# Kernel tuning notes

Hardware: AMD Instinct MI355X
Metric: run time of the kernel (lower is better)

The kernel has to match this reference:

```python
import jax, jax.numpy as jnp
import numpy as np
from jax import lax

K = 7            # cfg.network.PSROI_BINS == pool_size
FEAT_STRIDE = 16
LAMDA = 0.1
D_PER_BIN = 8    # feature channels per position-sensitive bin -> C = K*K*8 = 392


def _bilinear(feat, y, x, extra_idx):
    """Bilinearly sample feat[H,W,...] at float coords (y,x); extra_idx are
    integer index arrays (broadcast to y.shape) selecting trailing feat axes."""
    H, W = feat.shape[0], feat.shape[1]
    y0f = jnp.floor(y); x0f = jnp.floor(x)
    wy = (y - y0f)[..., None]
    wx = (x - x0f)[..., None]
    y0 = jnp.clip(y0f.astype(jnp.int32), 0, H - 1)
    y1 = jnp.clip(y0f.astype(jnp.int32) + 1, 0, H - 1)
    x0 = jnp.clip(x0f.astype(jnp.int32), 0, W - 1)
    x1 = jnp.clip(x0f.astype(jnp.int32) + 1, 0, W - 1)
    def g(yi, xi):
        return feat[(yi, xi) + extra_idx]
    return ((1 - wy) * (1 - wx) * g(y0, x0) + (1 - wy) * wx * g(y0, x1)
            + wy * (1 - wx) * g(y1, x0) + wy * wx * g(y1, x1))


def ps_roi(f, rois, k, feat_stride, offsets=None):
    """Position-sensitive RoI pooling. f: [H,W,C] with C = k*k*D (bin-major
    channel layout). rois: [N,5] (batch, x1, y1, x2, y2) in image coords.
    offsets (optional): [N, k*k, G, 2] per-bin, per-channel-group (x,y) shifts
    in image coords. Returns [N, D, k, k]."""
    H, W, C = f.shape
    N = rois.shape[0]
    kk = k * k
    D = C // kk
    x1 = rois[:, 1] / feat_stride
    y1 = rois[:, 2] / feat_stride
    x2 = (rois[:, 3] + 1.0) / feat_stride
    y2 = (rois[:, 4] + 1.0) / feat_stride
    bw = (x2 - x1) / k  # [N]
    bh = (y2 - y1) / k
    jj = jnp.tile(jnp.arange(k, dtype=f.dtype), k)     # bin = i*k + j
    ii = jnp.repeat(jnp.arange(k, dtype=f.dtype), k)
    cx = x1[:, None] + (jj + 0.5) * bw[:, None]        # [N, kk] bin centers
    cy = y1[:, None] + (ii + 0.5) * bh[:, None]
    bins = jnp.arange(kk, dtype=jnp.int32)
    if offsets is None:
        feat = f.reshape(H, W, kk, D)
        b = jnp.broadcast_to(bins, (N, kk))
        vals = _bilinear(feat, cy, cx, (b,))           # [N, kk, D]
    else:
        G = offsets.shape[2]
        cxg = cx[:, :, None] + offsets[..., 0] / feat_stride  # [N, kk, G]
        cyg = cy[:, :, None] + offsets[..., 1] / feat_stride
        feat = f.reshape(H, W, kk, G, D // G)
        b = jnp.broadcast_to(bins[None, :, None], (N, kk, G))
        g = jnp.broadcast_to(jnp.arange(G, dtype=jnp.int32)[None, None, :], (N, kk, G))
        vals = _bilinear(feat, cyg, cxg, (b, g))       # [N, kk, G, D//G]
        vals = vals.reshape(N, kk, D)
    return jnp.transpose(vals.reshape(N, k, k, D), (0, 3, 1, 2))  # [N, D, k, k]


def setup_inputs():
    key = jax.random.key(0)
    kf, kw, k1, k2 = jax.random.split(key, 4)
    H = W = 128
    C = K * K * D_PER_BIN
    N = 2048
    features = jax.random.normal(kf, (1, H, W, C), jnp.float32)
    conv_w = jax.random.normal(kw, (3, 3, C, 2 * 4 * K * K), jnp.float32) * 0.01
    img = float(H * FEAT_STRIDE)
    xy1 = jax.random.uniform(k1, (N, 2), minval=0.0, maxval=img * 0.6)
    wh = jax.random.uniform(k2, (N, 2), minval=32.0, maxval=img * 0.4)
    xy2 = jnp.minimum(xy1 + wh, img - 1.0)
    rois = jnp.concatenate([jnp.zeros((N, 1)), xy1[:, :1], xy1[:, 1:], xy2[:, :1], xy2[:, 1:]], axis=1).astype(jnp.float32)
    return {"features": features, "rois": rois, "conv_w": conv_w}


def reference(features, rois, conv_w):
    # offset branch: 3x3 conv (no bias) -> PS-RoI pool -> scale by lamda*roi size
    offset_map = lax.conv_general_dilated(features, conv_w, (1, 1), 'SAME',
                                          dimension_numbers=('NHWC', 'HWIO', 'NHWC'))
    off = ps_roi(offset_map[0], rois, K, FEAT_STRIDE)          # [N, 8, K, K]
    N = off.shape[0]
    off = off.reshape(N, -1, 2, K, K)                          # [N, 4, 2, K, K]
    off = jnp.transpose(off, (2, 3, 4, 1, 0))                  # [2, K, K, 4, N]
    roi_w = rois[:, 3] - rois[:, 1] + 1.0
    roi_h = rois[:, 4] - rois[:, 2] + 1.0
    off = jnp.stack((off[0] * roi_w * LAMDA, off[1] * roi_h * LAMDA), axis=0)
    off = jnp.transpose(off, (4, 1, 2, 3, 0))                  # [N, K, K, 4, 2]
    off = off.reshape(N, K * K, -1, 2)                         # [N, kk, 4, 2]
    # deformable PS-RoI pooling of the features with predicted offsets
    return ps_roi(features[0], rois, K, FEAT_STRIDE, offsets=off)  # [N, 8, K, K]
```

## Files before the change

### kernel.cpp

```cpp
#include <hip/hip_runtime.h>
#include <cstddef>
#include <cstdint>

#define HH    128
#define WW    128
#define CC    392
#define NPIX  (HH*WW)
#define NROI  2048
#define PSK   7
#define NBIN  49
#define LAMDA 0.1f

#define CPAD      448
#define HPAD      130
#define NPADCO    512
#define SEGSTRIDE (9*CPAD)
#define BKK       64

#define FBM 64
#define FBN 64
#define FBK 32

typedef _Float16 half8   __attribute__((ext_vector_type(8)));
typedef float    floatx4 __attribute__((ext_vector_type(4)));

__device__ __forceinline__ void async_ld16(const _Float16* g, _Float16* l) {
  __builtin_amdgcn_global_load_lds((const __attribute__((address_space(1))) void*)g,
                                   (__attribute__((address_space(3))) void*)l,
                                   16, 0, 0);
}

__global__ __launch_bounds__(256)
void conv_f_kernel(const float* __restrict__ F, _Float16* __restrict__ Fh) {
  const int idx = blockIdx.x * 256 + threadIdx.x;
  const int total = HPAD * HPAD * (CPAD / 8);
  if (idx >= total) return;
  const int p  = idx / (CPAD / 8);
  const int cg = idx - p * (CPAD / 8);
  const int c  = cg * 8;
  const int py = p / HPAD;
  const int px = p - py * HPAD;
  half8 h;
#pragma unroll
  for (int i = 0; i < 8; ++i) h[i] = (_Float16)0.f;
  if (py >= 1 && py <= HH && px >= 1 && px <= WW && c < CC) {
    const float* src = F + ((size_t)(py - 1) * WW + (px - 1)) * CC + c;
    const float4 v0 = *(const float4*)src;
    const float4 v1 = *(const float4*)(src + 4);
    h[0] = (_Float16)v0.x; h[1] = (_Float16)v0.y;
    h[2] = (_Float16)v0.z; h[3] = (_Float16)v0.w;
    h[4] = (_Float16)v1.x; h[5] = (_Float16)v1.y;
    h[6] = (_Float16)v1.z; h[7] = (_Float16)v1.w;
  }
  *(half8*)(Fh + (size_t)p * CPAD + c) = h;
}

__global__ __launch_bounds__(256)
void conv_w_kernel(const float* __restrict__ Wt, _Float16* __restrict__ Bth) {
  __shared__ float tile[32][33];
  const int bid = blockIdx.x;
  const int seg = bid / (14 * 16);
  const int rem = bid - seg * (14 * 16);
  const int cit = rem / 16;
  const int cot = rem - cit * 16;
  const int ci0 = cit * 32, co0 = cot * 32;
  const int t = threadIdx.x;
#pragma unroll
  for (int i = 0; i < 4; ++i) {
    const int idx = t + i * 256;
    const int lr = idx >> 5;
    const int lc = idx & 31;
    const int ci = ci0 + lr, co = co0 + lc;
    float v = 0.f;
    if (ci < CC && co < CC) v = Wt[((size_t)seg * CC + ci) * CC + co];
    tile[lr][lc] = v;
  }
  __syncthreads();
#pragma unroll
  for (int i = 0; i < 4; ++i) {
    const int idx = t + i * 256;
    const int lr = idx >> 5;
    const int lc = idx & 31;
    Bth[(size_t)(co0 + lr) * SEGSTRIDE + seg * CPAD + ci0 + lc] = (_Float16)tile[lc][lr];
  }
}

__global__ __launch_bounds__(256, 2)
void conv_mfma_kernel(const _Float16* __restrict__ Fh, const _Float16* __restrict__ Bth,
                      _Float16* __restrict__ OM) {
  __shared__ __align__(16) _Float16 As[128 * BKK];
  __shared__ __align__(16) _Float16 Bs[128 * BKK];

  const int t = threadIdx.x;
  const int L = t & 63;
  const int w = t >> 6;
  const int row0 = blockIdx.x * 128;
  const int col0 = blockIdx.y * 128;

  const int srow = L >> 3;
  const int kofs = ((L & 7) ^ srow) * 8;

  const int ya = row0 >> 7;
  const int nbase = col0 + w * 32 + srow;

  const int wm = (w >> 1) * 64;
  const int wn = (w & 1) * 64;
  const int fr = L & 15;
  const int quad = L >> 4;
  const int pg0 = (quad ^ (fr & 7)) * 8;
  const int pg1 = ((4 + quad) ^ (fr & 7)) * 8;

  floatx4 acc[4][4];
#pragma unroll
  for (int i = 0; i < 4; ++i)
#pragma unroll
    for (int j = 0; j < 4; ++j) {
      floatx4 z = {0.f, 0.f, 0.f, 0.f};
      acc[i][j] = z;
    }

  for (int seg = 0; seg < 9; ++seg) {
    const int dy = seg / 3 - 1;
    const int dx = seg - (seg / 3) * 3 - 1;
    const int fy = ya + 1 + dy;
    const _Float16* gArow = Fh + ((size_t)fy * HPAD + (1 + dx)) * CPAD + kofs;
    const _Float16* gB = Bth + (size_t)nbase * SEGSTRIDE + seg * CPAD + kofs;

    for (int it = 0; it < 7; ++it) {
      const int cb = it * BKK;
#pragma unroll
      for (int j = 0; j < 4; ++j) {
        const int xr = w * 32 + j * 8 + srow;
        async_ld16(gArow + (size_t)xr * CPAD + cb, &As[(w * 32 + j * 8) * BKK]);
      }
#pragma unroll
      for (int j = 0; j < 4; ++j) {
        async_ld16(gB + (size_t)(j * 8) * SEGSTRIDE + cb, &Bs[(w * 32 + j * 8) * BKK]);
      }
      __syncthreads();

      half8 a0[4], a1[4], b0[4], b1[4];
#pragma unroll
      for (int mt = 0; mt < 4; ++mt) {
        const int rb = (wm + mt * 16 + fr) * BKK;
        a0[mt] = *(const half8*)(&As[rb + pg0]);
        a1[mt] = *(const half8*)(&As[rb + pg1]);
      }
#pragma unroll
      for (int nt = 0; nt < 4; ++nt) {
        const int rb = (wn + nt * 16 + fr) * BKK;
        b0[nt] = *(const half8*)(&Bs[rb + pg0]);
        b1[nt] = *(const half8*)(&Bs[rb + pg1]);
      }
#pragma unroll
      for (int mt = 0; mt < 4; ++mt)
#pragma unroll
        for (int nt = 0; nt < 4; ++nt)
          acc[mt][nt] = __builtin_amdgcn_mfma_f32_16x16x32_f16(a0[mt], b0[nt], acc[mt][nt], 0, 0, 0);
#pragma unroll
      for (int mt = 0; mt < 4; ++mt)
#pragma unroll
        for (int nt = 0; nt < 4; ++nt)
          acc[mt][nt] = __builtin_amdgcn_mfma_f32_16x16x32_f16(a1[mt], b1[nt], acc[mt][nt], 0, 0, 0);
      __syncthreads();
    }
  }

#pragma unroll
  for (int mt = 0; mt < 4; ++mt) {
    const int rbase = row0 + wm + mt * 16 + quad * 4;
#pragma unroll
    for (int nt = 0; nt < 4; ++nt) {
      const int col = col0 + wn + nt * 16 + fr;
      if (col < CC) {
#pragma unroll
        for (int r = 0; r < 4; ++r)
          OM[(size_t)(rbase + r) * CC + col] = (_Float16)acc[mt][nt][r];
      }
    }
  }
}

__global__ __launch_bounds__(256)
void conv3x3_kernel(const float* __restrict__ F, const float* __restrict__ Wt,
                    float* __restrict__ OM) {
  __shared__ float Asf[FBK][FBM + 4];
  __shared__ float Bsf[FBK][FBN + 4];

  const int t = threadIdx.x;
  const int ty = t >> 4;
  const int tx = t & 15;
  const int row0 = blockIdx.x * FBM;
  const int col0 = blockIdx.y * FBN;

  float acc[4][4];
#pragma unroll
  for (int i = 0; i < 4; ++i)
#pragma unroll
    for (int j = 0; j < 4; ++j) acc[i][j] = 0.f;

  for (int kc = 0; kc < 117; ++kc) {
    const int seg   = kc / 13;
    const int cbase = (kc - seg * 13) * FBK;
    const int dy    = seg / 3 - 1;
    const int dx    = seg - (seg / 3) * 3 - 1;

#pragma unroll
    for (int rep = 0; rep < (FBM * FBK) / 256; ++rep) {
      const int idx = t + rep * 256;
      const int r  = idx >> 5;
      const int lk = idx & 31;
      const int m  = row0 + r;
      const int y  = m >> 7, x = m & 127;
      const int yy = y + dy, xx = x + dx;
      const int ci = cbase + lk;
      float v = 0.f;
      if ((unsigned)yy < HH && (unsigned)xx < WW && ci < CC)
        v = F[((size_t)(yy * WW + xx)) * CC + ci];
      Asf[lk][r] = v;
    }
#pragma unroll
    for (int rep = 0; rep < (FBK * FBN) / 256; ++rep) {
      const int idx = t + rep * 256;
      const int lk  = idx >> 6;
      const int nn  = idx & 63;
      const int ci  = cbase + lk;
      const int col = col0 + nn;
      float v = 0.f;
      if (ci < CC && col < CC)
        v = Wt[((size_t)(seg * CC + ci)) * CC + col];
      Bsf[lk][nn] = v;
    }
    __syncthreads();

#pragma unroll
    for (int lk = 0; lk < FBK; ++lk) {
      const float4 a4 = *(const float4*)(&Asf[lk][ty * 4]);
      const float4 b4 = *(const float4*)(&Bsf[lk][tx * 4]);
      const float av[4] = {a4.x, a4.y, a4.z, a4.w};
      const float bv[4] = {b4.x, b4.y, b4.z, b4.w};
#pragma unroll
      for (int i = 0; i < 4; ++i)
#pragma unroll
        for (int j = 0; j < 4; ++j)
          acc[i][j] = fmaf(av[i], bv[j], acc[i][j]);
    }
    __syncthreads();
  }

  const int col = col0 + tx * 4;
  if (col < CC) {
#pragma unroll
    for (int i = 0; i < 4; ++i) {
      float4 v = make_float4(acc[i][0], acc[i][1], acc[i][2], acc[i][3]);
      *(float4*)(&OM[((size_t)(row0 + ty * 4 + i)) * CC + col]) = v;
    }
  }
}

__device__ __forceinline__ void bilin_setup(float y, float x,
                                            int& iy0, int& iy1, int& ix0, int& ix1,
                                            float& w00, float& w01, float& w10, float& w11) {
  const float y0f = floorf(y), x0f = floorf(x);
  const float wy = y - y0f, wx = x - x0f;
  const int a = (int)y0f, b = (int)x0f;
  iy0 = min(max(a, 0), HH - 1);
  iy1 = min(max(a + 1, 0), HH - 1);
  ix0 = min(max(b, 0), WW - 1);
  ix1 = min(max(b + 1, 0), WW - 1);
  w00 = (1.f - wy) * (1.f - wx);
  w01 = (1.f - wy) * wx;
  w10 = wy * (1.f - wx);
  w11 = wy * wx;
}

template <typename TOM>
__global__ __launch_bounds__(256)
void psroi_pool_kernel(const float* __restrict__ F, const float* __restrict__ R,
                       const TOM* __restrict__ OM, float* __restrict__ out) {
  const int tid = blockIdx.x * 256 + threadIdx.x;
  if (tid >= NROI * NBIN * 4) return;
  const int g  = tid & 3;
  const int nb = tid >> 2;
  const int n  = nb / NBIN;
  const int b  = nb - n * NBIN;
  const int bi = b / PSK;
  const int bj = b - bi * PSK;

  const float rx1 = R[n * 5 + 1], ry1 = R[n * 5 + 2];
  const float rx2 = R[n * 5 + 3], ry2 = R[n * 5 + 4];

  const float x1 = rx1 * (1.f / 16.f);
  const float y1 = ry1 * (1.f / 16.f);
  const float x2 = (rx2 + 1.f) * (1.f / 16.f);
  const float y2 = (ry2 + 1.f) * (1.f / 16.f);
  const float bw = (x2 - x1) * (1.f / 7.f);
  const float bh = (y2 - y1) * (1.f / 7.f);
  const float cx = x1 + ((float)bj + 0.5f) * bw;
  const float cy = y1 + ((float)bi + 0.5f) * bh;

  int iy0, iy1, ix0, ix1;
  float w00, w01, w10, w11;
  bilin_setup(cy, cx, iy0, iy1, ix0, ix1, w00, w01, w10, w11);

  const size_t c0 = (size_t)b * 8 + 2 * g;
  const size_t s00 = (size_t)(iy0 * WW + ix0) * CC + c0;
  const size_t s01 = (size_t)(iy0 * WW + ix1) * CC + c0;
  const size_t s10 = (size_t)(iy1 * WW + ix0) * CC + c0;
  const size_t s11 = (size_t)(iy1 * WW + ix1) * CC + c0;

  const float ox = w00 * (float)OM[s00]     + w01 * (float)OM[s01]
                 + w10 * (float)OM[s10]     + w11 * (float)OM[s11];
  const float oy = w00 * (float)OM[s00 + 1] + w01 * (float)OM[s01 + 1]
                 + w10 * (float)OM[s10 + 1] + w11 * (float)OM[s11 + 1];

  const float roiw = rx2 - rx1 + 1.f;
  const float roih = ry2 - ry1 + 1.f;
  const float sx = cx + ox * roiw * (LAMDA / 16.f);
  const float sy = cy + oy * roih * (LAMDA / 16.f);

  int jy0, jy1, jx0, jx1;
  float u00, u01, u10, u11;
  bilin_setup(sy, sx, jy0, jy1, jx0, jx1, u00, u01, u10, u11);

  const float2 q00 = *(const float2*)(F + (size_t)(jy0 * WW + jx0) * CC + c0);
  const float2 q01 = *(const float2*)(F + (size_t)(jy0 * WW + jx1) * CC + c0);
  const float2 q10 = *(const float2*)(F + (size_t)(jy1 * WW + jx0) * CC + c0);
  const float2 q11 = *(const float2*)(F + (size_t)(jy1 * WW + jx1) * CC + c0);

  const float v0 = u00 * q00.x + u01 * q01.x + u10 * q10.x + u11 * q11.x;
  const float v1 = u00 * q00.y + u01 * q01.y + u10 * q10.y + u11 * q11.y;

  out[((size_t)n * 8 + 2 * g + 0) * NBIN + b] = v0;
  out[((size_t)n * 8 + 2 * g + 1) * NBIN + b] = v1;
}

extern "C" void kernel_launch(void* const* d_in, const int* in_sizes, int n_in,
                              void* d_out, int out_size, void* d_ws, size_t ws_size,
                              hipStream_t stream) {
  const float* F  = (const float*)d_in[0];
  const float* R  = (const float*)d_in[1];
  const float* Wt = (const float*)d_in[2];
  float* out = (float*)d_out;

  const size_t omBytes  = (size_t)NPIX * CC * sizeof(_Float16);
  const size_t fhBytes  = (size_t)HPAD * HPAD * CPAD * sizeof(_Float16);
  const size_t bthBytes = (size_t)NPADCO * SEGSTRIDE * sizeof(_Float16);
  const size_t need = omBytes + fhBytes + bthBytes;

  const int totalPool = NROI * NBIN * 4;

  if (ws_size >= need) {
    _Float16* OM  = (_Float16*)d_ws;
    _Float16* Fh  = (_Float16*)((char*)d_ws + omBytes);
    _Float16* Bth = (_Float16*)((char*)d_ws + omBytes + fhBytes);

    const int fTotal = HPAD * HPAD * (CPAD / 8);
    conv_f_kernel<<<(fTotal + 255) / 256, 256, 0, stream>>>(F, Fh);
    conv_w_kernel<<<9 * 14 * 16, 256, 0, stream>>>(Wt, Bth);

    dim3 g(NPIX / 128, NPADCO / 128);
    conv_mfma_kernel<<<g, 256, 0, stream>>>(Fh, Bth, OM);

    psroi_pool_kernel<_Float16><<<(totalPool + 255) / 256, 256, 0, stream>>>(F, R, OM, out);
  } else {
    float* OM = (float*)d_ws;
    dim3 cgrid(NPIX / FBM, (CC + FBN - 1) / FBN);
    conv3x3_kernel<<<cgrid, 256, 0, stream>>>(F, Wt, OM);
    psroi_pool_kernel<float><<<(totalPool + 255) / 256, 256, 0, stream>>>(F, R, OM, out);
  }
}
```

Before: 166.4 us.

## Shrink conv N-tile padding, merge prep kernels, pool from fp16 features

Reduces output-channel padding from 512 to 448 and halves the MFMA tile width to 64 columns, which cuts wasted MMA work and doubles the grid while raising the occupancy hint. It also merges the feature and weight conversion kernels into one launch, flattens the seg/k loops, and makes the pooling kernel read half2 offset values and the fp16 padded feature copy instead of fp32 features. Narrower tiles reduce A-tile reuse per block, and sampling from fp16 features adds rounding error in the final output.

```diff
diff --git a/kernel.cpp b/kernel.cpp
--- a/kernel.cpp
+++ b/kernel.cpp
@@ -13,7 +13,7 @@
 
 #define CPAD      448
 #define HPAD      130
-#define NPADCO    512
+#define NPADCO    448
 #define SEGSTRIDE (9*CPAD)
 #define BKK       64
 
@@ -22,6 +22,7 @@
 #define FBK 32
 
 typedef _Float16 half8   __attribute__((ext_vector_type(8)));
+typedef _Float16 half2v  __attribute__((ext_vector_type(2)));
 typedef float    floatx4 __attribute__((ext_vector_type(4)));
 
 __device__ __forceinline__ void async_ld16(const _Float16* g, _Float16* l) {
@@ -30,147 +31,150 @@
                                    16, 0, 0);
 }
 
+#define FPREP ((HPAD * HPAD * (CPAD / 8) + 255) / 256)
+#define WPREP (9 * 14 * 14)
+
 __global__ __launch_bounds__(256)
-void conv_f_kernel(const float* __restrict__ F, _Float16* __restrict__ Fh) {
-  const int idx = blockIdx.x * 256 + threadIdx.x;
-  const int total = HPAD * HPAD * (CPAD / 8);
-  if (idx >= total) return;
-  const int p  = idx / (CPAD / 8);
-  const int cg = idx - p * (CPAD / 8);
-  const int c  = cg * 8;
-  const int py = p / HPAD;
-  const int px = p - py * HPAD;
-  half8 h;
-#pragma unroll
-  for (int i = 0; i < 8; ++i) h[i] = (_Float16)0.f;
-  if (py >= 1 && py <= HH && px >= 1 && px <= WW && c < CC) {
-    const float* src = F + ((size_t)(py - 1) * WW + (px - 1)) * CC + c;
-    const float4 v0 = *(const float4*)src;
-    const float4 v1 = *(const float4*)(src + 4);
-    h[0] = (_Float16)v0.x; h[1] = (_Float16)v0.y;
-    h[2] = (_Float16)v0.z; h[3] = (_Float16)v0.w;
-    h[4] = (_Float16)v1.x; h[5] = (_Float16)v1.y;
-    h[6] = (_Float16)v1.z; h[7] = (_Float16)v1.w;
-  }
-  *(half8*)(Fh + (size_t)p * CPAD + c) = h;
-}
-
-__global__ __launch_bounds__(256)
-void conv_w_kernel(const float* __restrict__ Wt, _Float16* __restrict__ Bth) {
+void prep_kernel(const float* __restrict__ F, const float* __restrict__ Wt,
+                 _Float16* __restrict__ Fh, _Float16* __restrict__ Bth) {
   __shared__ float tile[32][33];
-  const int bid = blockIdx.x;
-  const int seg = bid / (14 * 16);
-  const int rem = bid - seg * (14 * 16);
-  const int cit = rem / 16;
-  const int cot = rem - cit * 16;
-  const int ci0 = cit * 32, co0 = cot * 32;
   const int t = threadIdx.x;
-#pragma unroll
-  for (int i = 0; i < 4; ++i) {
-    const int idx = t + i * 256;
-    const int lr = idx >> 5;
-    const int lc = idx & 31;
-    const int ci = ci0 + lr, co = co0 + lc;
-    float v = 0.f;
-    if (ci < CC && co < CC) v = Wt[((size_t)seg * CC + ci) * CC + co];
-    tile[lr][lc] = v;
-  }
-  __syncthreads();
-#pragma unroll
-  for (int i = 0; i < 4; ++i) {
-    const int idx = t + i * 256;
-    const int lr = idx >> 5;
-    const int lc = idx & 31;
-    Bth[(size_t)(co0 + lr) * SEGSTRIDE + seg * CPAD + ci0 + lc] = (_Float16)tile[lc][lr];
-  }
-}
-
-__global__ __launch_bounds__(256, 2)
+  if (blockIdx.x < FPREP) {
+    const int idx = blockIdx.x * 256 + t;
+    const int total = HPAD * HPAD * (CPAD / 8);
+    if (idx >= total) return;
+    const int p  = idx / (CPAD / 8);
+    const int cg = idx - p * (CPAD / 8);
+    const int c  = cg * 8;
+    const int py = p / HPAD;
+    const int px = p - py * HPAD;
+    half8 h;
+#pragma unroll
+    for (int i = 0; i < 8; ++i) h[i] = (_Float16)0.f;
+    if (py >= 1 && py <= HH && px >= 1 && px <= WW && c < CC) {
+      const float* src = F + ((size_t)(py - 1) * WW + (px - 1)) * CC + c;
+      const float4 v0 = *(const float4*)src;
+      const float4 v1 = *(const float4*)(src + 4);
+      h[0] = (_Float16)v0.x; h[1] = (_Float16)v0.y;
+      h[2] = (_Float16)v0.z; h[3] = (_Float16)v0.w;
+      h[4] = (_Float16)v1.x; h[5] = (_Float16)v1.y;
+      h[6] = (_Float16)v1.z; h[7] = (_Float16)v1.w;
+    }
+    *(half8*)(Fh + (size_t)p * CPAD + c) = h;
+  } else {
+    const int bid = blockIdx.x - FPREP;
+    const int seg = bid / (14 * 14);
+    const int rem = bid - seg * (14 * 14);
+    const int cit = rem / 14;
+    const int cot = rem - cit * 14;
+    const int ci0 = cit * 32, co0 = cot * 32;
+#pragma unroll
+    for (int i = 0; i < 4; ++i) {
+      const int idx = t + i * 256;
+      const int lr = idx >> 5;
+      const int lc = idx & 31;
+      const int ci = ci0 + lr, co = co0 + lc;
+      float v = 0.f;
+      if (ci < CC && co < CC) v = Wt[((size_t)seg * CC + ci) * CC + co];
+      tile[lr][lc] = v;
+    }
+    __syncthreads();
+#pragma unroll
+    for (int i = 0; i < 4; ++i) {
+      const int idx = t + i * 256;
+      const int lr = idx >> 5;
+      const int lc = idx & 31;
+      Bth[(size_t)(co0 + lr) * SEGSTRIDE + seg * CPAD + ci0 + lc] = (_Float16)tile[lc][lr];
+    }
+  }
+}
+
+__global__ __launch_bounds__(256, 4)
 void conv_mfma_kernel(const _Float16* __restrict__ Fh, const _Float16* __restrict__ Bth,
                       _Float16* __restrict__ OM) {
   __shared__ __align__(16) _Float16 As[128 * BKK];
-  __shared__ __align__(16) _Float16 Bs[128 * BKK];
+  __shared__ __align__(16) _Float16 Bs[64 * BKK];
 
   const int t = threadIdx.x;
   const int L = t & 63;
   const int w = t >> 6;
   const int row0 = blockIdx.x * 128;
-  const int col0 = blockIdx.y * 128;
+  const int col0 = blockIdx.y * 64;
 
   const int srow = L >> 3;
   const int kofs = ((L & 7) ^ srow) * 8;
 
   const int ya = row0 >> 7;
-  const int nbase = col0 + w * 32 + srow;
+  const int nbase = col0 + w * 16 + srow;
 
   const int wm = (w >> 1) * 64;
-  const int wn = (w & 1) * 64;
+  const int wn = (w & 1) * 32;
   const int fr = L & 15;
   const int quad = L >> 4;
   const int pg0 = (quad ^ (fr & 7)) * 8;
   const int pg1 = ((4 + quad) ^ (fr & 7)) * 8;
 
-  floatx4 acc[4][4];
+  floatx4 acc[4][2];
 #pragma unroll
   for (int i = 0; i < 4; ++i)
 #pragma unroll
-    for (int j = 0; j < 4; ++j) {
+    for (int j = 0; j < 2; ++j) {
       floatx4 z = {0.f, 0.f, 0.f, 0.f};
       acc[i][j] = z;
     }
 
-  for (int seg = 0; seg < 9; ++seg) {
+  for (int q = 0; q < 63; ++q) {
+    const int seg = q / 7;
+    const int it  = q - seg * 7;
     const int dy = seg / 3 - 1;
     const int dx = seg - (seg / 3) * 3 - 1;
     const int fy = ya + 1 + dy;
-    const _Float16* gArow = Fh + ((size_t)fy * HPAD + (1 + dx)) * CPAD + kofs;
-    const _Float16* gB = Bth + (size_t)nbase * SEGSTRIDE + seg * CPAD + kofs;
-
-    for (int it = 0; it < 7; ++it) {
-      const int cb = it * BKK;
-#pragma unroll
-      for (int j = 0; j < 4; ++j) {
-        const int xr = w * 32 + j * 8 + srow;
-        async_ld16(gArow + (size_t)xr * CPAD + cb, &As[(w * 32 + j * 8) * BKK]);
-      }
-#pragma unroll
-      for (int j = 0; j < 4; ++j) {
-        async_ld16(gB + (size_t)(j * 8) * SEGSTRIDE + cb, &Bs[(w * 32 + j * 8) * BKK]);
-      }
-      __syncthreads();
-
-      half8 a0[4], a1[4], b0[4], b1[4];
-#pragma unroll
-      for (int mt = 0; mt < 4; ++mt) {
-        const int rb = (wm + mt * 16 + fr) * BKK;
-        a0[mt] = *(const half8*)(&As[rb + pg0]);
-        a1[mt] = *(const half8*)(&As[rb + pg1]);
-      }
-#pragma unroll
-      for (int nt = 0; nt < 4; ++nt) {
-        const int rb = (wn + nt * 16 + fr) * BKK;
-        b0[nt] = *(const half8*)(&Bs[rb + pg0]);
-        b1[nt] = *(const half8*)(&Bs[rb + pg1]);
-      }
-#pragma unroll
-      for (int mt = 0; mt < 4; ++mt)
-#pragma unroll
-        for (int nt = 0; nt < 4; ++nt)
-          acc[mt][nt] = __builtin_amdgcn_mfma_f32_16x16x32_f16(a0[mt], b0[nt], acc[mt][nt], 0, 0, 0);
-#pragma unroll
-      for (int mt = 0; mt < 4; ++mt)
-#pragma unroll
-        for (int nt = 0; nt < 4; ++nt)
-          acc[mt][nt] = __builtin_amdgcn_mfma_f32_16x16x32_f16(a1[mt], b1[nt], acc[mt][nt], 0, 0, 0);
-      __syncthreads();
-    }
+    const int cb = it * BKK;
+    const _Float16* gArow = Fh + ((size_t)fy * HPAD + (1 + dx)) * CPAD + kofs + cb;
+    const _Float16* gB = Bth + (size_t)nbase * SEGSTRIDE + seg * CPAD + kofs + cb;
+
+#pragma unroll
+    for (int j = 0; j < 4; ++j) {
+      const int xr = w * 32 + j * 8 + srow;
+      async_ld16(gArow + (size_t)xr * CPAD, &As[(w * 32 + j * 8) * BKK]);
+    }
+#pragma unroll
+    for (int j = 0; j < 2; ++j) {
+      async_ld16(gB + (size_t)(j * 8) * SEGSTRIDE, &Bs[(w * 16 + j * 8) * BKK]);
+    }
+    __syncthreads();
+
+    half8 a0[4], a1[4], b0[2], b1[2];
+#pragma unroll
+    for (int mt = 0; mt < 4; ++mt) {
+      const int rb = (wm + mt * 16 + fr) * BKK;
+      a0[mt] = *(const half8*)(&As[rb + pg0]);
+      a1[mt] = *(const half8*)(&As[rb + pg1]);
+    }
+#pragma unroll
+    for (int nt = 0; nt < 2; ++nt) {
+      const int rb = (wn + nt * 16 + fr) * BKK;
+      b0[nt] = *(const half8*)(&Bs[rb + pg0]);
+      b1[nt] = *(const half8*)(&Bs[rb + pg1]);
+    }
+#pragma unroll
+    for (int mt = 0; mt < 4; ++mt)
+#pragma unroll
+      for (int nt = 0; nt < 2; ++nt)
+        acc[mt][nt] = __builtin_amdgcn_mfma_f32_16x16x32_f16(a0[mt], b0[nt], acc[mt][nt], 0, 0, 0);
+#pragma unroll
+    for (int mt = 0; mt < 4; ++mt)
+#pragma unroll
+      for (int nt = 0; nt < 2; ++nt)
+        acc[mt][nt] = __builtin_amdgcn_mfma_f32_16x16x32_f16(a1[mt], b1[nt], acc[mt][nt], 0, 0, 0);
+    __syncthreads();
   }
 
 #pragma unroll
   for (int mt = 0; mt < 4; ++mt) {
     const int rbase = row0 + wm + mt * 16 + quad * 4;
 #pragma unroll
-    for (int nt = 0; nt < 4; ++nt) {
+    for (int nt = 0; nt < 2; ++nt) {
       const int col = col0 + wn + nt * 16 + fr;
       if (col < CC) {
 #pragma unroll
@@ -274,10 +278,25 @@
   w11 = wy * wx;
 }
 
-template <typename TOM>
+__device__ __forceinline__ void roi_geom(const float* R, int n, int bi, int bj,
+                                         float& cx, float& cy, float& sxs, float& sys) {
+  const float rx1 = R[n * 5 + 1], ry1 = R[n * 5 + 2];
+  const float rx2 = R[n * 5 + 3], ry2 = R[n * 5 + 4];
+  const float x1 = rx1 * (1.f / 16.f);
+  const float y1 = ry1 * (1.f / 16.f);
+  const float x2 = (rx2 + 1.f) * (1.f / 16.f);
+  const float y2 = (ry2 + 1.f) * (1.f / 16.f);
+  const float bw = (x2 - x1) * (1.f / 7.f);
+  const float bh = (y2 - y1) * (1.f / 7.f);
+  cx = x1 + ((float)bj + 0.5f) * bw;
+  cy = y1 + ((float)bi + 0.5f) * bh;
+  sxs = (rx2 - rx1 + 1.f) * (LAMDA / 16.f);
+  sys = (ry2 - ry1 + 1.f) * (LAMDA / 16.f);
+}
+
 __global__ __launch_bounds__(256)
-void psroi_pool_kernel(const float* __restrict__ F, const float* __restrict__ R,
-                       const TOM* __restrict__ OM, float* __restrict__ out) {
+void psroi_pool_f16_kernel(const _Float16* __restrict__ Fh, const float* __restrict__ R,
+                           const _Float16* __restrict__ OM, float* __restrict__ out) {
   const int tid = blockIdx.x * 256 + threadIdx.x;
   if (tid >= NROI * NBIN * 4) return;
   const int g  = tid & 3;
@@ -287,37 +306,75 @@
   const int bi = b / PSK;
   const int bj = b - bi * PSK;
 
-  const float rx1 = R[n * 5 + 1], ry1 = R[n * 5 + 2];
-  const float rx2 = R[n * 5 + 3], ry2 = R[n * 5 + 4];
-
-  const float x1 = rx1 * (1.f / 16.f);
-  const float y1 = ry1 * (1.f / 16.f);
-  const float x2 = (rx2 + 1.f) * (1.f / 16.f);
-  const float y2 = (ry2 + 1.f) * (1.f / 16.f);
-  const float bw = (x2 - x1) * (1.f / 7.f);
-  const float bh = (y2 - y1) * (1.f / 7.f);
-  const float cx = x1 + ((float)bj + 0.5f) * bw;
-  const float cy = y1 + ((float)bi + 0.5f) * bh;
+  float cx, cy, sxs, sys;
+  roi_geom(R, n, bi, bj, cx, cy, sxs, sys);
 
   int iy0, iy1, ix0, ix1;
   float w00, w01, w10, w11;
   bilin_setup(cy, cx, iy0, iy1, ix0, ix1, w00, w01, w10, w11);
 
   const size_t c0 = (size_t)b * 8 + 2 * g;
-  const size_t s00 = (size_t)(iy0 * WW + ix0) * CC + c0;
-  const size_t s01 = (size_t)(iy0 * WW + ix1) * CC + c0;
-  const size_t s10 = (size_t)(iy1 * WW + ix0) * CC + c0;
-  const size_t s11 = (size_t)(iy1 * WW + ix1) * CC + c0;
-
-  const float ox = w00 * (float)OM[s00]     + w01 * (float)OM[s01]
-                 + w10 * (float)OM[s10]     + w11 * (float)OM[s11];
-  const float oy = w00 * (float)OM[s00 + 1] + w01 * (float)OM[s01 + 1]
-                 + w10 * (float)OM[s10 + 1] + w11 * (float)OM[s11 + 1];
-
-  const float roiw = rx2 - rx1 + 1.f;
-  const float roih = ry2 - ry1 + 1.f;
-  const float sx = cx + ox * roiw * (LAMDA / 16.f);
-  const float sy = cy + oy * roih * (LAMDA / 16.f);
+  const half2v m00 = *(const half2v*)(OM + (size_t)(iy0 * WW + ix0) * CC + c0);
+  const half2v m01 = *(const half2v*)(OM + (size_t)(iy0 * WW + ix1) * CC + c0);
+  const half2v m10 = *(const half2v*)(OM + (size_t)(iy1 * WW + ix0) * CC + c0);
+  const half2v m11 = *(const half2v*)(OM + (size_t)(iy1 * WW + ix1) * CC + c0);
+
+  const float ox = w00 * (float)m00[0] + w01 * (float)m01[0]
+                 + w10 * (float)m10[0] + w11 * (float)m11[0];
+  const float oy = w00 * (float)m00[1] + w01 * (float)m01[1]
+                 + w10 * (float)m10[1] + w11 * (float)m11[1];
+
+  const float sx = cx + ox * sxs;
+  const float sy = cy + oy * sys;
+
+  int jy0, jy1, jx0, jx1;
+  float u00, u01, u10, u11;
+  bilin_setup(sy, sx, jy0, jy1, jx0, jx1, u00, u01, u10, u11);
+
+  const half2v q00 = *(const half2v*)(Fh + ((size_t)(jy0 + 1) * HPAD + (jx0 + 1)) * CPAD + c0);
+  const half2v q01 = *(const half2v*)(Fh + ((size_t)(jy0 + 1) * HPAD + (jx1 + 1)) * CPAD + c0);
+  const half2v q10 = *(const half2v*)(Fh + ((size_t)(jy1 + 1) * HPAD + (jx0 + 1)) * CPAD + c0);
+  const half2v q11 = *(const half2v*)(Fh + ((size_t)(jy1 + 1) * HPAD + (jx1 + 1)) * CPAD + c0);
+
+  const float v0 = u00 * (float)q00[0] + u01 * (float)q01[0]
+                 + u10 * (float)q10[0] + u11 * (float)q11[0];
+  const float v1 = u00 * (float)q00[1] + u01 * (float)q01[1]
+                 + u10 * (float)q10[1] + u11 * (float)q11[1];
+
+  out[((size_t)n * 8 + 2 * g + 0) * NBIN + b] = v0;
+  out[((size_t)n * 8 + 2 * g + 1) * NBIN + b] = v1;
+}
+
+__global__ __launch_bounds__(256)
+void psroi_pool_f32_kernel(const float* __restrict__ F, const float* __restrict__ R,
+                           const float* __restrict__ OM, float* __restrict__ out) {
+  const int tid = blockIdx.x * 256 + threadIdx.x;
+  if (tid >= NROI * NBIN * 4) return;
+  const int g  = tid & 3;
+  const int nb = tid >> 2;
+  const int n  = nb / NBIN;
+  const int b  = nb - n * NBIN;
+  const int bi = b / PSK;
+  const int bj = b - bi * PSK;
+
+  float cx, cy, sxs, sys;
+  roi_geom(R, n, bi, bj, cx, cy, sxs, sys);
+
+  int iy0, iy1, ix0, ix1;
+  float w00, w01, w10, w11;
+  bilin_setup(cy, cx, iy0, iy1, ix0, ix1, w00, w01, w10, w11);
+
+  const size_t c0 = (size_t)b * 8 + 2 * g;
+  const float2 m00 = *(const float2*)(OM + (size_t)(iy0 * WW + ix0) * CC + c0);
+  const float2 m01 = *(const float2*)(OM + (size_t)(iy0 * WW + ix1) * CC + c0);
+  const float2 m10 = *(const float2*)(OM + (size_t)(iy1 * WW + ix0) * CC + c0);
+  const float2 m11 = *(const float2*)(OM + (size_t)(iy1 * WW + ix1) * CC + c0);
+
+  const float ox = w00 * m00.x + w01 * m01.x + w10 * m10.x + w11 * m11.x;
+  const float oy = w00 * m00.y + w01 * m01.y + w10 * m10.y + w11 * m11.y;
+
+  const float sx = cx + ox * sxs;
+  const float sy = cy + oy * sys;
 
   int jy0, jy1, jx0, jx1;
   float u00, u01, u10, u11;
@@ -349,24 +406,23 @@
   const size_t need = omBytes + fhBytes + bthBytes;
 
   const int totalPool = NROI * NBIN * 4;
+  const int poolGrid = (totalPool + 255) / 256;
 
   if (ws_size >= need) {
     _Float16* OM  = (_Float16*)d_ws;
     _Float16* Fh  = (_Float16*)((char*)d_ws + omBytes);
-    _Float16* Bth = (_Float16*)((char*)d_ws + omBytes + fhBytes);
-
-    const int fTotal = HPAD * HPAD * (CPAD / 8);
-    conv_f_kernel<<<(fTotal + 255) / 256, 256, 0, stream>>>(F, Fh);
-    conv_w_kernel<<<9 * 14 * 16, 256, 0, stream>>>(Wt, Bth);
-
-    dim3 g(NPIX / 128, NPADCO / 128);
+    _Float16* Bth = Fh + (size_t)HPAD * HPAD * CPAD;
+
+    prep_kernel<<<FPREP + WPREP, 256, 0, stream>>>(F, Wt, Fh, Bth);
+
+    dim3 g(NPIX / 128, NPADCO / 64);
     conv_mfma_kernel<<<g, 256, 0, stream>>>(Fh, Bth, OM);
 
-    psroi_pool_kernel<_Float16><<<(totalPool + 255) / 256, 256, 0, stream>>>(F, R, OM, out);
+    psroi_pool_f16_kernel<<<poolGrid, 256, 0, stream>>>(Fh, R, OM, out);
   } else {
-    float* OM = (float*)d_ws;
+    float* OMf = (float*)d_ws;
     dim3 cgrid(NPIX / FBM, (CC + FBN - 1) / FBN);
-    conv3x3_kernel<<<cgrid, 256, 0, stream>>>(F, Wt, OM);
-    psroi_pool_kernel<float><<<(totalPool + 255) / 256, 256, 0, stream>>>(F, R, OM, out);
-  }
-}
+    conv3x3_kernel<<<cgrid, 256, 0, stream>>>(F, Wt, OMf);
+    psroi_pool_f32_kernel<<<poolGrid, 256, 0, stream>>>(F, R, OMf, out);
+  }
+}
```

Measured after the change: 164.6 us. About the same (-1.1%).
